# Kernel optimization log

Measured on AMD Instinct MI355X. Metric: run time of the kernel, lower is better.

## Reference

```python
import jax, jax.numpy as jnp
import numpy as np

N_EMBD = 768
HEAD_SIZE = 64
B, T = 32, 1024


def setup_inputs() -> dict:
    key = jax.random.key(0)
    k1, k2, k3, k4 = jax.random.split(key, 4)
    x = jax.random.normal(k1, (B, T, N_EMBD), dtype=jnp.float32)
    Wq = jax.random.normal(k2, (N_EMBD, HEAD_SIZE), dtype=jnp.float32) * 0.02
    Wk = jax.random.normal(k3, (N_EMBD, HEAD_SIZE), dtype=jnp.float32) * 0.02
    Wv = jax.random.normal(k4, (N_EMBD, HEAD_SIZE), dtype=jnp.float32) * 0.02
    return {"x": x, "Wq": Wq, "Wk": Wk, "Wv": Wv}


def _apply_rope(q, k):
    # q, k: [B, T, D]; interleaved (even/odd) RoPE exactly as the torch source
    seq_len, dim = q.shape[-2], q.shape[-1]
    pos = jnp.arange(seq_len, dtype=jnp.float32)[:, None]                      # [T, 1]
    div_term = jnp.exp(jnp.arange(0, dim, 2, dtype=jnp.float32) * (-jnp.log(10000.0) / dim))  # [D/2]
    sin_emb = jnp.sin(pos * div_term)                                          # [T, D/2]
    cos_emb = jnp.cos(pos * div_term)                                          # [T, D/2]

    def rot(t):
        te, to = t[..., ::2], t[..., 1::2]
        re = te * cos_emb - to * sin_emb
        ro = te * sin_emb + to * cos_emb
        # interleave back: [..., T, D/2, 2] -> [..., T, D]
        return jnp.stack([re, ro], axis=-1).reshape(t.shape)

    return rot(q), rot(k)


def reference(x, Wq, Wk, Wv):
    Bx, Tx, C = x.shape  # C == n_embd
    q = x @ Wq  # [B, T, D]
    k = x @ Wk
    v = x @ Wv
    q, k = _apply_rope(q, k)
    # NOTE: source scales by C**-0.5 where C = n_embd, not head_size
    wei = jnp.einsum('btd,bsd->bts', q, k) * (C ** -0.5)  # [B, T, T]
    causal = jnp.tril(jnp.ones((Tx, Tx), dtype=bool))
    wei = jnp.where(causal, wei, -jnp.inf)
    wei = jax.nn.softmax(wei, axis=-1)
    # dropout is identity in eval mode
    out = jnp.einsum('bts,bsd->btd', wei, v)  # [B, T, D]
    return out
```

## Files before the change

### kernel.cpp

```cpp
#include <hip/hip_runtime.h>
#include <cmath>

#define B 32
#define T 1024
#define CDIM 768
#define D 64
#define SCALE 0.03608439182435161f
#define XSTR 72

typedef short bf16x8 __attribute__((ext_vector_type(8)));
typedef float f32x4 __attribute__((ext_vector_type(4)));
typedef float f32x16 __attribute__((ext_vector_type(16)));
typedef unsigned short u16x8 __attribute__((ext_vector_type(8)));

__device__ inline ushort f2bf(float f) {
  union { float f; unsigned u; } v{f};
  unsigned r = (v.u + 0x7FFFu + ((v.u >> 16) & 1u)) >> 16;
  return (ushort)r;
}

__device__ __forceinline__ void gll16(const void* g, void* l) {
  __builtin_amdgcn_global_load_lds(
      (const __attribute__((address_space(1))) void*)g,
      (__attribute__((address_space(3))) void*)l, 16, 0, 0);
}

__global__ __launch_bounds__(256) void wt_prep(
    const float* __restrict__ Wq, const float* __restrict__ Wk,
    const float* __restrict__ Wv, ushort* __restrict__ Wt)
{
  const int n   = blockIdx.x;
  const int sel = n >> 6, col = n & 63;
  const float* W = (sel == 0) ? Wq : (sel == 1) ? Wk : Wv;
  const float sc = (sel == 0) ? SCALE : 1.f;
  const int swz = (n & 7) << 3;
  for (int k = threadIdx.x; k < CDIM; k += 256) {
    const int s = k >> 6, kl = k & 63;
    Wt[(size_t)(s * 192 + n) * 64 + (kl ^ swz)] = f2bf(W[(size_t)k * D + col] * sc);
  }
}

__global__ __launch_bounds__(256) void proj_mfma(
    const float* __restrict__ x,
    const ushort* __restrict__ Wt,
    ushort* __restrict__ qkv)
{
  const int t    = threadIdx.x;
  const int lane = t & 63;
  const int wid  = t >> 6;
  const int ln32 = lane & 31;
  const int half = lane >> 5;
  const int mw   = wid & 1;
  const int nh   = wid >> 1;
  const int row0 = blockIdx.x * 64;

  __shared__ float  Xf[2][64 * 64];
  __shared__ ushort Wl[192 * 64];

  f32x16 acc[3];
  #pragma unroll
  for (int nt = 0; nt < 3; ++nt)
    #pragma unroll
    for (int rg = 0; rg < 16; ++rg) acc[nt][rg] = 0.f;

  const float* xb0 = x + (size_t)row0 * CDIM;

  auto stage_X = [&](int s, int bu) {
    #pragma unroll
    for (int i = 0; i < 4; ++i) {
      const int lin = i * 256 + wid * 64 + lane;
      const int row = lin >> 4, sl = lin & 15;
      const int c   = sl ^ (row & 15);
      gll16(xb0 + (size_t)row * CDIM + s * 64 + c * 4,
            &Xf[bu][(i * 256 + wid * 64) * 4]);
    }
  };
  auto stage_W = [&](int s) {
    const ushort* wb = Wt + (size_t)s * (192 * 64);
    #pragma unroll
    for (int i = 0; i < 6; ++i) {
      const int lin = i * 256 + wid * 64 + lane;
      gll16(wb + lin * 8, &Wl[(i * 256 + wid * 64) * 8]);
    }
  };

  const int xr  = mw * 32 + ln32;
  const int xsw = xr & 15;

  stage_X(0, 0);
  #pragma unroll
  for (int s = 0; s < CDIM / 64; ++s) {
    const int bu = s & 1;
    stage_W(s);
    if (s + 1 < CDIM / 64) {
      stage_X(s + 1, bu ^ 1);
      asm volatile("s_waitcnt vmcnt(4)" ::: "memory");
    } else {
      asm volatile("s_waitcnt vmcnt(0)" ::: "memory");
    }
    __builtin_amdgcn_s_barrier();

    #pragma unroll
    for (int kk = 0; kk < 4; ++kk) {
      const int c0 = kk * 4 + half * 2;
      f32x4 f0 = *(const f32x4*)&Xf[bu][xr * 64 + ((c0 ^ xsw) << 2)];
      f32x4 f1 = *(const f32x4*)&Xf[bu][xr * 64 + (((c0 + 1) ^ xsw) << 2)];
      union { ushort u[8]; bf16x8 v; } af;
      af.u[0] = f2bf(f0[0]); af.u[1] = f2bf(f0[1]);
      af.u[2] = f2bf(f0[2]); af.u[3] = f2bf(f0[3]);
      af.u[4] = f2bf(f1[0]); af.u[5] = f2bf(f1[1]);
      af.u[6] = f2bf(f1[2]); af.u[7] = f2bf(f1[3]);
      #pragma unroll
      for (int nt = 0; nt < 3; ++nt) {
        const int wr = nh * 96 + nt * 32 + ln32;
        const int cc = (kk * 2 + half) ^ (wr & 7);
        bf16x8 bb = *(const bf16x8*)&Wl[wr * 64 + (cc << 3)];
        acc[nt] = __builtin_amdgcn_mfma_f32_32x32x16_bf16(af.v, bb, acc[nt], 0, 0, 0);
      }
    }
    __builtin_amdgcn_s_barrier();
  }

  #pragma unroll
  for (int nt = 0; nt < 3; ++nt) {
    const int n   = nh * 96 + nt * 32 + ln32;
    const int sel = n >> 6;
    const int d   = n & 63;
    ushort* outb = qkv + (size_t)sel * (B * T * D);
    if (sel < 2) {
      const float freq = __expf((float)(d & 62) * (-0.14391156855801f));
      const float sgn  = (d & 1) ? 1.f : -1.f;
      #pragma unroll
      for (int reg = 0; reg < 16; ++reg) {
        int rowg = row0 + mw * 32 + (reg & 3) + 8 * (reg >> 2) + 4 * half;
        float sv, cv;
        __sincosf((float)(rowg & (T - 1)) * freq, &sv, &cv);
        float val = acc[nt][reg];
        float partner = __shfl_xor(val, 1, 64);
        outb[(size_t)rowg * D + d] = f2bf(fmaf(sgn * partner, sv, val * cv));
      }
    } else {
      #pragma unroll
      for (int reg = 0; reg < 16; ++reg) {
        int rowg = row0 + mw * 32 + (reg & 3) + 8 * (reg >> 2) + 4 * half;
        outb[(size_t)rowg * D + d] = f2bf(acc[nt][reg]);
      }
    }
  }
}

__global__ __launch_bounds__(256) void attn_mfma(
    const ushort* __restrict__ qg,
    const ushort* __restrict__ kg,
    const ushort* __restrict__ vg,
    float* __restrict__ out)
{
  const int t    = threadIdx.x;
  const int lane = t & 63;
  const int wid  = t >> 6;
  const int ln16 = lane & 15;
  const int quad = lane >> 4;
  const int l    = (int)blockIdx.x;
  const int b    = l & 31;
  const int r    = l >> 5;
  const int qt   = (r < 8) ? r : 23 - r;

  __shared__ ushort Ks[2][64 * XSTR];
  __shared__ ushort Vt[2][64 * XSTR];
  __shared__ ushort Pl[64 * XSTR];

  bf16x8 qf[2];
  {
    const ushort* qrow = qg + (size_t)(b * T + qt * 64 + wid * 16 + ln16) * D;
    qf[0] = *(const bf16x8*)(qrow + quad * 8);
    qf[1] = *(const bf16x8*)(qrow + quad * 8 + 32);
  }

  f32x4 O[4];
  #pragma unroll
  for (int nt = 0; nt < 4; ++nt) O[nt] = (f32x4){0.f, 0.f, 0.f, 0.f};
  float l_sum = 0.f;

  const int kb = t & 15, db = t >> 4;
  const int d0 = db * 4, kk0 = kb * 4;

  u16x8  kp[2];
  ushort4 vp[4];
  auto load_kv = [&](int kt) {
    #pragma unroll
    for (int i = 0; i < 2; ++i) {
      int slot = i * 256 + t, row = slot >> 3, dblk = slot & 7;
      kp[i] = *(const u16x8*)(kg + (size_t)(b * T + kt * 64 + row) * D + dblk * 8);
    }
    #pragma unroll
    for (int i = 0; i < 4; ++i)
      vp[i] = *(const ushort4*)(vg + (size_t)(b * T + kt * 64 + kk0 + i) * D + d0);
  };

  load_kv(0);
  int buf = 0;
  for (int kt = 0; kt <= qt; ++kt) {
    #pragma unroll
    for (int i = 0; i < 2; ++i) {
      int slot = i * 256 + t, row = slot >> 3, dblk = slot & 7;
      *(u16x8*)&Ks[buf][row * XSTR + dblk * 8] = kp[i];
    }
    const ushort* vpe = (const ushort*)vp;
    #pragma unroll
    for (int j = 0; j < 4; ++j) {
      ushort4 c;
      c.x = vpe[0 * 4 + j]; c.y = vpe[1 * 4 + j];
      c.z = vpe[2 * 4 + j]; c.w = vpe[3 * 4 + j];
      *(ushort4*)&Vt[buf][(d0 + j) * XSTR + kk0] = c;
    }
    __syncthreads();
    if (kt < qt) load_kv(kt + 1);

    f32x4 s[4];
    #pragma unroll
    for (int mt = 0; mt < 4; ++mt) s[mt] = (f32x4){0.f, 0.f, 0.f, 0.f};
    #pragma unroll
    for (int ks = 0; ks < 2; ++ks)
      #pragma unroll
      for (int mt = 0; mt < 4; ++mt) {
        bf16x8 kf = *(const bf16x8*)&Ks[buf][(mt * 16 + ln16) * XSTR + quad * 8 + ks * 32];
        s[mt] = __builtin_amdgcn_mfma_f32_16x16x32_bf16(kf, qf[ks], s[mt], 0, 0, 0);
      }

    if (kt == qt) {
      const int ql = wid * 16 + ln16;
      #pragma unroll
      for (int mt = 0; mt < 4; ++mt)
        #pragma unroll
        for (int reg = 0; reg < 4; ++reg)
          if (mt * 16 + quad * 4 + reg > ql) s[mt][reg] = -1e30f;
    }

    float psum = 0.f;
    #pragma unroll
    for (int mt = 0; mt < 4; ++mt) {
      float p0 = __expf(s[mt][0]), p1 = __expf(s[mt][1]);
      float p2 = __expf(s[mt][2]), p3 = __expf(s[mt][3]);
      psum += (p0 + p1) + (p2 + p3);
      ushort4 pk;
      pk.x = f2bf(p0); pk.y = f2bf(p1); pk.z = f2bf(p2); pk.w = f2bf(p3);
      *(ushort4*)&Pl[(wid * 16 + ln16) * XSTR + mt * 16 + quad * 4] = pk;
    }
    psum += __shfl_xor(psum, 16, 64);
    psum += __shfl_xor(psum, 32, 64);
    l_sum += psum;

    bf16x8 pa[2];
    pa[0] = *(const bf16x8*)&Pl[(wid * 16 + ln16) * XSTR + quad * 8];
    pa[1] = *(const bf16x8*)&Pl[(wid * 16 + ln16) * XSTR + quad * 8 + 32];
    #pragma unroll
    for (int ks = 0; ks < 2; ++ks)
      #pragma unroll
      for (int nt = 0; nt < 4; ++nt) {
        bf16x8 vf = *(const bf16x8*)&Vt[buf][(nt * 16 + ln16) * XSTR + quad * 8 + ks * 32];
        O[nt] = __builtin_amdgcn_mfma_f32_16x16x32_bf16(pa[ks], vf, O[nt], 0, 0, 0);
      }
    buf ^= 1;
  }

  float inv = 1.f / l_sum;
  #pragma unroll
  for (int reg = 0; reg < 4; ++reg) {
    float iv = __shfl(inv, quad * 4 + reg, 64);
    size_t row = (size_t)(b * T + qt * 64 + wid * 16 + quad * 4 + reg) * D;
    #pragma unroll
    for (int nt = 0; nt < 4; ++nt)
      out[row + nt * 16 + ln16] = O[nt][reg] * iv;
  }
}

extern "C" void kernel_launch(void* const* d_in, const int* in_sizes, int n_in,
                              void* d_out, int out_size, void* d_ws, size_t ws_size,
                              hipStream_t stream) {
  const float* x  = (const float*)d_in[0];
  const float* Wq = (const float*)d_in[1];
  const float* Wk = (const float*)d_in[2];
  const float* Wv = (const float*)d_in[3];
  float* outp = (float*)d_out;

  ushort* qkv = (ushort*)d_ws;
  ushort* Wt  = qkv + (size_t)3 * B * T * D;

  wt_prep<<<dim3(192), dim3(256), 0, stream>>>(Wq, Wk, Wv, Wt);
  proj_mfma<<<dim3((B * T) / 64), dim3(256), 0, stream>>>(x, Wt, qkv);
  attn_mfma<<<dim3(T / 64 * B), dim3(256), 0, stream>>>(
      qkv, qkv + (size_t)B * T * D, qkv + 2 * (size_t)B * T * D, outp);
}
```

Before: 182.6 us.

## Split long causal query tiles across two KV ranges and merge partials

Query tiles 8-15 now have their KV loop split into two halves, each run by its own block, which raises the grid from 512 to 768 blocks. The halves write unnormalized O and row sums to workspace, and a new merge kernel adds them and normalizes. The goal is to shorten the longest per-block critical path and balance load across CUs under the causal mask. It costs an extra kernel launch and a round trip of partial outputs through global memory, and launch bounds now ask for 3 blocks per CU. The merge assumes both halves share a common max, since the softmax here appears to be computed without a running max.

```diff
diff --git a/kernel.cpp b/kernel.cpp
--- a/kernel.cpp
+++ b/kernel.cpp
@@ -149,11 +149,13 @@
   }
 }
 
-__global__ __launch_bounds__(256) void attn_mfma(
+__global__ __launch_bounds__(256, 3) void attn_mfma(
     const ushort* __restrict__ qg,
     const ushort* __restrict__ kg,
     const ushort* __restrict__ vg,
-    float* __restrict__ out)
+    float* __restrict__ out,
+    float* __restrict__ Op,
+    float* __restrict__ Lp)
 {
   const int t    = threadIdx.x;
   const int lane = t & 63;
@@ -162,8 +164,11 @@
   const int quad = lane >> 4;
   const int l    = (int)blockIdx.x;
   const int b    = l & 31;
-  const int r    = l >> 5;
-  const int qt   = (r < 8) ? r : 23 - r;
+  const int j    = l >> 5;
+  const int qt   = (j < 16) ? j : 31 - j;
+  const int kt0  = (j < 16) ? 0 : 8;
+  const int ktN  = (j < 8) ? j : (j < 16 ? 7 : qt);
+  const int hf   = (j >= 16);
 
   __shared__ ushort Ks[2][64 * XSTR];
   __shared__ ushort Vt[2][64 * XSTR];
@@ -197,9 +202,9 @@
       vp[i] = *(const ushort4*)(vg + (size_t)(b * T + kt * 64 + kk0 + i) * D + d0);
   };
 
-  load_kv(0);
+  load_kv(kt0);
   int buf = 0;
-  for (int kt = 0; kt <= qt; ++kt) {
+  for (int kt = kt0; kt <= ktN; ++kt) {
     #pragma unroll
     for (int i = 0; i < 2; ++i) {
       int slot = i * 256 + t, row = slot >> 3, dblk = slot & 7;
@@ -207,14 +212,14 @@
     }
     const ushort* vpe = (const ushort*)vp;
     #pragma unroll
-    for (int j = 0; j < 4; ++j) {
+    for (int jj = 0; jj < 4; ++jj) {
       ushort4 c;
-      c.x = vpe[0 * 4 + j]; c.y = vpe[1 * 4 + j];
-      c.z = vpe[2 * 4 + j]; c.w = vpe[3 * 4 + j];
-      *(ushort4*)&Vt[buf][(d0 + j) * XSTR + kk0] = c;
+      c.x = vpe[0 * 4 + jj]; c.y = vpe[1 * 4 + jj];
+      c.z = vpe[2 * 4 + jj]; c.w = vpe[3 * 4 + jj];
+      *(ushort4*)&Vt[buf][(d0 + jj) * XSTR + kk0] = c;
     }
     __syncthreads();
-    if (kt < qt) load_kv(kt + 1);
+    if (kt < ktN) load_kv(kt + 1);
 
     f32x4 s[4];
     #pragma unroll
@@ -263,14 +268,45 @@
     buf ^= 1;
   }
 
-  float inv = 1.f / l_sum;
-  #pragma unroll
-  for (int reg = 0; reg < 4; ++reg) {
-    float iv = __shfl(inv, quad * 4 + reg, 64);
-    size_t row = (size_t)(b * T + qt * 64 + wid * 16 + quad * 4 + reg) * D;
-    #pragma unroll
-    for (int nt = 0; nt < 4; ++nt)
-      out[row + nt * 16 + ln16] = O[nt][reg] * iv;
+  if (j < 8) {
+    float inv = 1.f / l_sum;
+    #pragma unroll
+    for (int reg = 0; reg < 4; ++reg) {
+      float iv = __shfl(inv, quad * 4 + reg, 64);
+      size_t row = (size_t)(b * T + qt * 64 + wid * 16 + quad * 4 + reg) * D;
+      #pragma unroll
+      for (int nt = 0; nt < 4; ++nt)
+        out[row + nt * 16 + ln16] = O[nt][reg] * iv;
+    }
+  } else {
+    float* Ob = Op + (size_t)(((b * 8 + (qt - 8)) * 2 + hf) * 4096);
+    #pragma unroll
+    for (int reg = 0; reg < 4; ++reg) {
+      const int row = wid * 16 + quad * 4 + reg;
+      #pragma unroll
+      for (int nt = 0; nt < 4; ++nt)
+        Ob[row * 64 + nt * 16 + ln16] = O[nt][reg];
+    }
+    if (quad == 0)
+      Lp[((b * 8 + (qt - 8)) * 2 + hf) * 64 + wid * 16 + ln16] = l_sum;
+  }
+}
+
+__global__ __launch_bounds__(256) void attn_merge(
+    const float* __restrict__ Op, const float* __restrict__ Lp,
+    float* __restrict__ out)
+{
+  const int blk = blockIdx.x;
+  const int b = blk & 31, qtb = blk >> 5;
+  const int qt = qtb + 8;
+  const float* Oa = Op + (size_t)((b * 8 + qtb) * 2) * 4096;
+  const float* Ob = Oa + 4096;
+  const float* La = Lp + (size_t)((b * 8 + qtb) * 2) * 64;
+  const float* Lb = La + 64;
+  for (int idx = threadIdx.x; idx < 4096; idx += 256) {
+    const int row = idx >> 6, d = idx & 63;
+    const float li = 1.f / (La[row] + Lb[row]);
+    out[(size_t)(b * T + qt * 64 + row) * D + d] = (Oa[idx] + Ob[idx]) * li;
   }
 }
 
@@ -285,9 +321,12 @@
 
   ushort* qkv = (ushort*)d_ws;
   ushort* Wt  = qkv + (size_t)3 * B * T * D;
+  float*  Op  = (float*)(Wt + (size_t)12 * 192 * 64);
+  float*  Lp  = Op + (size_t)32 * 8 * 2 * 64 * 64;
 
   wt_prep<<<dim3(192), dim3(256), 0, stream>>>(Wq, Wk, Wv, Wt);
   proj_mfma<<<dim3((B * T) / 64), dim3(256), 0, stream>>>(x, Wt, qkv);
-  attn_mfma<<<dim3(T / 64 * B), dim3(256), 0, stream>>>(
-      qkv, qkv + (size_t)B * T * D, qkv + 2 * (size_t)B * T * D, outp);
-}
+  attn_mfma<<<dim3(768), dim3(256), 0, stream>>>(
+      qkv, qkv + (size_t)B * T * D, qkv + 2 * (size_t)B * T * D, outp, Op, Lp);
+  attn_merge<<<dim3(256), dim3(256), 0, stream>>>(Op, Lp, outp);
+}
```

Result: no change. 182.8 us (+0.1%).
